# Kernel tuning notes

Hardware: AMD Instinct MI355X
Metric: run time of the kernel (lower is better)

Reference implementation:

```python
import jax, jax.numpy as jnp
import numpy as np

B, T, D = 16384, 3, 512   # batch, task_num, input_dim
G = T + 1                  # expert groups (idx 0 shared)
NE = 4                     # experts per group
H, E = 512, 256            # expert hidden, expert output dim (layers=[512,256])
GH = 256                   # gate hidden
TH, TO = 128, 64           # tower hidden / output dims


def setup_inputs() -> dict:
    key = jax.random.key(0)
    ks = jax.random.split(key, 14)
    s = 0.02
    return {
        "inputs": jax.random.normal(ks[0], (B, G, D), jnp.float32),
        # expert MLPs: [group, expert, ...]
        "expert_W1": jax.random.normal(ks[1], (G, NE, D, H), jnp.float32) * s,
        "expert_b1": jnp.zeros((G, NE, H), jnp.float32),
        "expert_W2": jax.random.normal(ks[2], (G, NE, H, E), jnp.float32) * s,
        "expert_b2": jnp.zeros((G, NE, E), jnp.float32),
        # per-task gates (softmax over G*NE experts)
        "gate_W1": jax.random.normal(ks[3], (T, D, GH), jnp.float32) * s,
        "gate_b1": jnp.zeros((T, GH), jnp.float32),
        "gate_W2": jax.random.normal(ks[4], (T, GH, G * NE), jnp.float32) * s,
        "gate_b2": jnp.zeros((T, G * NE), jnp.float32),
        # per-task towers (is_last=True)
        "tower_W1": jax.random.normal(ks[5], (T, E, TH), jnp.float32) * s,
        "tower_b1": jnp.zeros((T, TH), jnp.float32),
        "tower_W2": jax.random.normal(ks[6], (T, TH, TO), jnp.float32) * s,
        "tower_b2": jnp.zeros((T, TO), jnp.float32),
    }


def reference(inputs, expert_W1, expert_b1, expert_W2, expert_b2,
              gate_W1, gate_b1, gate_W2, gate_b2,
              tower_W1, tower_b1, tower_W2, tower_b2):
    b = inputs.shape[0]
    g, ne = expert_W1.shape[0], expert_W1.shape[1]
    t_num = gate_W1.shape[0]

    # All expert groups in one batched einsum: [B, G, NE, E]
    h1 = jax.nn.relu(jnp.einsum('bgd,gndh->bgnh', inputs, expert_W1) + expert_b1)
    emb = jnp.einsum('bgnh,gnhe->bgne', h1, expert_W2) + expert_b2

    # Task gates on (task input + shared input): softmax over G*NE experts
    gin = inputs[:, 1:, :] + inputs[:, :1, :]                      # [B, T, D]
    gh = jax.nn.relu(jnp.einsum('btd,tdh->bth', gin, gate_W1) + gate_b1)
    gw = jax.nn.softmax(jnp.einsum('bth,thk->btk', gh, gate_W2) + gate_b2, axis=-1)  # [B,T,G*NE]

    emb_sg = jax.lax.stop_gradient(emb)
    group_ids = jnp.arange(g)
    outs = []
    for t in range(t_num):
        # gradient flows only through shared group (0) and own group (t+1)
        keep = (group_ids == 0) | (group_ids == t + 1)              # [G]
        masked = jnp.where(keep[None, :, None, None], emb, emb_sg)  # [B,G,NE,E]
        agg = jnp.einsum('bk,bke->be', gw[:, t], masked.reshape(b, g * ne, -1))  # [B,E]
        th = jax.nn.relu(agg @ tower_W1[t] + tower_b1[t])
        outs.append(th @ tower_W2[t] + tower_b2[t])                 # [B,TO]
    return jnp.concatenate(outs, axis=1)                           # [B, T*TO]
```

## Files before the change

kernel.cpp:

```cpp
#include <hip/hip_runtime.h>
#include <math.h>

#define B_N  16384
#define T_N  3
#define D_N  512
#define G_N  4
#define NE_N 4
#define H_N  512
#define E_N  256
#define GH_N 256
#define K16  16
#define TH_N 128
#define TO_N 64

typedef __attribute__((ext_vector_type(8))) short short8;
typedef __attribute__((ext_vector_type(4))) float floatx4;

__device__ __forceinline__ unsigned short f2bf(float f) {
    union { float f; unsigned u; } v; v.f = f;
    unsigned r = (v.u + 0x7fffu + ((v.u >> 16) & 1u)) >> 16;
    return (unsigned short)r;
}
__device__ __forceinline__ float bf2f(unsigned short h) {
    union { unsigned u; float f; } v; v.u = ((unsigned)h) << 16;
    return v.f;
}
__device__ __forceinline__ unsigned pack2(float lo, float hi) {
    return ((unsigned)f2bf(hi) << 16) | (unsigned)f2bf(lo);
}

typedef const __attribute__((address_space(1))) void gvoid_t;
typedef __attribute__((address_space(3))) void lvoid_t;

#if __has_builtin(__builtin_amdgcn_global_load_lds)
#define HAVE_GLL 1
__device__ __forceinline__ void load_lds16(const void* g, void* l) {
    __builtin_amdgcn_global_load_lds((gvoid_t*)g, (lvoid_t*)l, 16, 0, 0);
}
#else
#define HAVE_GLL 0
#endif

__global__ __launch_bounds__(256) void convert_inputs(
    const float* __restrict__ x, unsigned short* __restrict__ xb,
    unsigned short* __restrict__ ginb)
{
    const long b = blockIdx.x;
    const int tid = threadIdx.x;
    const float* xr = x + b * (G_N * D_N);
    unsigned short* xo = xb + b * (G_N * D_N);
    unsigned short* go = ginb + b * (T_N * D_N);
    float2 v0 = *(const float2*)&xr[tid * 2];
    *(unsigned*)&xo[tid * 2] = pack2(v0.x, v0.y);
    #pragma unroll
    for (int g = 1; g < G_N; ++g) {
        float2 v = *(const float2*)&xr[g * D_N + tid * 2];
        *(unsigned*)&xo[g * D_N + tid * 2] = pack2(v.x, v.y);
        *(unsigned*)&go[(g - 1) * D_N + tid * 2] = pack2(v.x + v0.x, v.y + v0.y);
    }
}

__global__ __launch_bounds__(256) void prep_kernel(
    const float* __restrict__ eW1, const float* __restrict__ eW2,
    const float* __restrict__ gW1, const float* __restrict__ tW1,
    const float* __restrict__ tW2,
    unsigned short* __restrict__ W1t, unsigned short* __restrict__ W2t,
    unsigned short* __restrict__ G1t, unsigned short* __restrict__ TW1t,
    unsigned short* __restrict__ TW2t,
    const float* __restrict__ x, unsigned short* __restrict__ xb,
    unsigned short* __restrict__ ginb)
{
    const int bid = blockIdx.x;
    if (bid < 6648) {
        const float* in; unsigned short* out; int K, N, nx, local;
        if (bid < 4096)      { in = eW1; out = W1t;  K = 512; N = 512; nx = 16; local = bid; }
        else if (bid < 6144) { in = eW2; out = W2t;  K = 512; N = 256; nx = 8;  local = bid - 4096; }
        else if (bid < 6528) { in = gW1; out = G1t;  K = 512; N = 256; nx = 8;  local = bid - 6144; }
        else if (bid < 6624) { in = tW1; out = TW1t; K = 256; N = 128; nx = 4;  local = bid - 6528; }
        else                 { in = tW2; out = TW2t; K = 128; N = 64;  nx = 2;  local = bid - 6624; }
        const int ny = K / 32;
        const int xt = local % nx;
        const int yt = (local / nx) % ny;
        const int z  = local / (nx * ny);
        __shared__ float tile[32][33];
        const int tx = threadIdx.x & 31, ty = threadIdx.x >> 5;
        const long zo = (long)z * K * N;
        const int n0 = xt * 32, k0 = yt * 32;
        #pragma unroll
        for (int i = 0; i < 4; ++i)
            tile[ty + 8 * i][tx] = in[zo + (long)(k0 + ty + 8 * i) * N + n0 + tx];
        __syncthreads();
        #pragma unroll
        for (int i = 0; i < 4; ++i)
            out[zo + (long)(n0 + ty + 8 * i) * K + k0 + tx] = f2bf(tile[tx][ty + 8 * i]);
    } else {
        const long b = bid - 6648;
        const int tid = threadIdx.x;
        const float* xr = x + b * (G_N * D_N);
        unsigned short* xo = xb + b * (G_N * D_N);
        unsigned short* go = ginb + b * (T_N * D_N);
        float2 v0 = *(const float2*)&xr[tid * 2];
        *(unsigned*)&xo[tid * 2] = pack2(v0.x, v0.y);
        #pragma unroll
        for (int g = 1; g < G_N; ++g) {
            float2 v = *(const float2*)&xr[g * D_N + tid * 2];
            *(unsigned*)&xo[g * D_N + tid * 2] = pack2(v.x, v.y);
            *(unsigned*)&go[(g - 1) * D_N + tid * 2] = pack2(v.x + v0.x, v.y + v0.y);
        }
    }
}

__global__ __launch_bounds__(256) void gate_fused(
    const unsigned short* __restrict__ ginb,
    const unsigned short* __restrict__ G1t,
    const float* __restrict__ gb1,
    const float* __restrict__ gW2,
    const float* __restrict__ gb2,
    float* __restrict__ gw)
{
    __shared__ __align__(16) unsigned short sm[40960];
    unsigned short* As  = sm;
    unsigned short* Bs  = sm + 4096;
    unsigned short* w2s = sm;
    unsigned short* ghs = sm + 8192;

    const int tid = threadIdx.x;
    const int t = blockIdx.y;
    const long b0 = (long)blockIdx.x * 128;
    const unsigned short* Ab = ginb + b0 * 1536 + (long)t * 512;

    const int lane16 = tid & 15;
    const int quad = (tid & 63) >> 4;
    const int wave = tid >> 6;
    const int wm = (wave >> 1) * 64;
    const int wn = (wave & 1) * 64;
    const int srow = tid >> 2;
    const int scol = (((tid & 3) ^ ((tid >> 3) & 3)) * 8);
    const int cw8 = ((quad ^ ((lane16 >> 1) & 3)) * 8);

    #pragma unroll
    for (int ncc = 0; ncc < 2; ++ncc) {
        const unsigned short* Bb = G1t + (long)t * 131072 + (long)(ncc * 128) * 512;
        floatx4 acc[4][4] = {};
        for (int k0 = 0; k0 < 512; k0 += 32) {
#if HAVE_GLL
            load_lds16(Ab + (long)srow * 1536 + k0 + scol, &As[tid * 8]);
            load_lds16(Ab + (long)(srow + 64) * 1536 + k0 + scol, &As[2048 + tid * 8]);
            load_lds16(Bb + (long)srow * 512 + k0 + scol, &Bs[tid * 8]);
            load_lds16(Bb + (long)(srow + 64) * 512 + k0 + scol, &Bs[2048 + tid * 8]);
#else
            *(uint4*)&As[tid * 8] = *(const uint4*)(Ab + (long)srow * 1536 + k0 + scol);
            *(uint4*)&As[2048 + tid * 8] = *(const uint4*)(Ab + (long)(srow + 64) * 1536 + k0 + scol);
            *(uint4*)&Bs[tid * 8] = *(const uint4*)(Bb + (long)srow * 512 + k0 + scol);
            *(uint4*)&Bs[2048 + tid * 8] = *(const uint4*)(Bb + (long)(srow + 64) * 512 + k0 + scol);
#endif
            __syncthreads();
            short8 a[4], b[4];
            #pragma unroll
            for (int mi = 0; mi < 4; ++mi)
                a[mi] = *(const short8*)&As[(wm + mi * 16 + lane16) * 32 + cw8];
            #pragma unroll
            for (int ni = 0; ni < 4; ++ni)
                b[ni] = *(const short8*)&Bs[(wn + ni * 16 + lane16) * 32 + cw8];
            #pragma unroll
            for (int mi = 0; mi < 4; ++mi)
                #pragma unroll
                for (int ni = 0; ni < 4; ++ni)
                    acc[mi][ni] = __builtin_amdgcn_mfma_f32_16x16x32_bf16(
                        a[mi], b[ni], acc[mi][ni], 0, 0, 0);
            __syncthreads();
        }
        #pragma unroll
        for (int mi = 0; mi < 4; ++mi) {
            #pragma unroll
            for (int ni = 0; ni < 4; ++ni) {
                const int col = ncc * 128 + wn + ni * 16 + lane16;
                const float bv = gb1[t * GH_N + col];
                #pragma unroll
                for (int r = 0; r < 4; ++r) {
                    const int row = wm + mi * 16 + quad * 4 + r;
                    const int pc = (col & 7) | ((((col >> 3) ^ (row & 7))) << 3);
                    ghs[row * 256 + pc] = f2bf(fmaxf(acc[mi][ni][r] + bv, 0.0f));
                }
            }
        }
    }
    {
        const float* W2p = gW2 + (long)t * (GH_N * K16);
        #pragma unroll
        for (int j = 0; j < 16; ++j)
            w2s[j * 264 + tid] = f2bf(W2p[(long)tid * K16 + j]);
    }
    __syncthreads();

    floatx4 ag[2] = {};
    #pragma unroll
    for (int kk = 0; kk < 8; ++kk) {
        short8 bfr = *(const short8*)&w2s[lane16 * 264 + kk * 32 + quad * 8];
        #pragma unroll
        for (int mi = 0; mi < 2; ++mi) {
            const int row = wave * 32 + mi * 16 + lane16;
            short8 afr = *(const short8*)&ghs[row * 256 + (((kk * 4 + quad) ^ (row & 7)) << 3)];
            ag[mi] = __builtin_amdgcn_mfma_f32_16x16x32_bf16(afr, bfr, ag[mi], 0, 0, 0);
        }
    }

    const float bb2 = gb2[t * K16 + lane16];
    #pragma unroll
    for (int mi = 0; mi < 2; ++mi) {
        float v[4], m = -1e30f;
        #pragma unroll
        for (int r = 0; r < 4; ++r) { v[r] = ag[mi][r] + bb2; }
        #pragma unroll
        for (int r = 0; r < 4; ++r) {
            float mv = v[r];
            #pragma unroll
            for (int d = 1; d < 16; d <<= 1) mv = fmaxf(mv, __shfl_xor(mv, d));
            float e = expf(v[r] - mv);
            float s = e;
            #pragma unroll
            for (int d = 1; d < 16; d <<= 1) s += __shfl_xor(s, d);
            const int row = wave * 32 + mi * 16 + quad * 4 + r;
            gw[(b0 + row) * (T_N * K16) + (long)t * K16 + lane16] = e / s;
        }
    }
}

__global__ __launch_bounds__(256, 2) void expert_fused(
    const unsigned short* __restrict__ xb,
    const unsigned short* __restrict__ W1t,
    const float* __restrict__ eb1,
    const unsigned short* __restrict__ W2t,
    const float* __restrict__ eb2,
    unsigned short* __restrict__ embb)
{
    __shared__ __align__(16) unsigned short sm[33792];
    unsigned short* As  = sm;
    unsigned short* Bs  = sm + 8192;
    unsigned short* h1s = sm + 16384;

    const int tid = threadIdx.x;
    const unsigned bid = blockIdx.x;
    const int e = ((bid & 7) << 1) | ((bid >> 3) & 1);
    const long m0 = (long)(bid >> 4) * 128;
    const int g = e >> 2;

    const unsigned short* Ab  = xb + m0 * 2048 + g * 512;
    const unsigned short* W1b = W1t + (long)e * (512 * 512);
    const unsigned short* W2b = W2t + (long)e * (256 * 512);

    const int lane16 = tid & 15;
    const int quad = (tid & 63) >> 4;
    const int wave = tid >> 6;
    const int wm  = (wave >> 1) * 64;
    const int wn  = (wave & 1) * 64;
    const int wn2 = (wave & 1) * 128;
    const int srow = tid >> 2;
    const int scolsw = (((tid & 3) ^ ((tid >> 3) & 3)) * 8);
    const int cw8 = ((quad ^ ((lane16 >> 1) & 3)) * 8);

    floatx4 acc2[4][8] = {};

    for (int nc = 0; nc < 4; ++nc) {
        const unsigned short* Bb = W1b + ((long)nc << 16);
        floatx4 acc[4][4] = {};
        for (int k0 = 0; k0 < 512; k0 += 64) {
            #pragma unroll
            for (int h = 0; h < 2; ++h) {
                const int kh = k0 + h * 32;
#if HAVE_GLL
                load_lds16(Ab + (long)srow * 2048 + kh + scolsw, &As[h * 4096 + tid * 8]);
                load_lds16(Ab + (long)(srow + 64) * 2048 + kh + scolsw, &As[h * 4096 + 2048 + tid * 8]);
                load_lds16(Bb + (long)srow * 512 + kh + scolsw, &Bs[h * 4096 + tid * 8]);
                load_lds16(Bb + (long)(srow + 64) * 512 + kh + scolsw, &Bs[h * 4096 + 2048 + tid * 8]);
#else
                *(uint4*)&As[h * 4096 + tid * 8] = *(const uint4*)(Ab + (long)srow * 2048 + kh + scolsw);
                *(uint4*)&As[h * 4096 + 2048 + tid * 8] = *(const uint4*)(Ab + (long)(srow + 64) * 2048 + kh + scolsw);
                *(uint4*)&Bs[h * 4096 + tid * 8] = *(const uint4*)(Bb + (long)srow * 512 + kh + scolsw);
                *(uint4*)&Bs[h * 4096 + 2048 + tid * 8] = *(const uint4*)(Bb + (long)(srow + 64) * 512 + kh + scolsw);
#endif
            }
            __syncthreads();
            #pragma unroll
            for (int h = 0; h < 2; ++h) {
                short8 b[4];
                #pragma unroll
                for (int ni = 0; ni < 4; ++ni)
                    b[ni] = *(const short8*)&Bs[h * 4096 + (wn + ni * 16 + lane16) * 32 + cw8];
                #pragma unroll
                for (int mi = 0; mi < 4; ++mi) {
                    short8 a = *(const short8*)&As[h * 4096 + (wm + mi * 16 + lane16) * 32 + cw8];
                    #pragma unroll
                    for (int ni = 0; ni < 4; ++ni)
                        acc[mi][ni] = __builtin_amdgcn_mfma_f32_16x16x32_bf16(
                            a, b[ni], acc[mi][ni], 0, 0, 0);
                }
            }
            __syncthreads();
        }
        #pragma unroll
        for (int mi = 0; mi < 4; ++mi) {
            #pragma unroll
            for (int ni = 0; ni < 4; ++ni) {
                const int col = wn + ni * 16 + lane16;
                const float bv = eb1[e * 512 + nc * 128 + col];
                #pragma unroll
                for (int r = 0; r < 4; ++r) {
                    const int row = wm + mi * 16 + quad * 4 + r;
                    h1s[row * 136 + col] = f2bf(fmaxf(acc[mi][ni][r] + bv, 0.0f));
                }
            }
        }
        __syncthreads();
        #pragma unroll
        for (int ks = 0; ks < 128; ks += 32) {
            #pragma unroll
            for (int i = 0; i < 4; ++i) {
#if HAVE_GLL
                load_lds16(W2b + (long)(srow + 64 * i) * 512 + nc * 128 + ks + scolsw,
                           &As[i * 2048 + tid * 8]);
#else
                *(uint4*)&As[i * 2048 + tid * 8] =
                    *(const uint4*)(W2b + (long)(srow + 64 * i) * 512 + nc * 128 + ks + scolsw);
#endif
            }
            __syncthreads();
            #pragma unroll
            for (int nh = 0; nh < 2; ++nh) {
                short8 b2[4];
                #pragma unroll
                for (int nj = 0; nj < 4; ++nj)
                    b2[nj] = *(const short8*)&As[(wn2 + nh * 64 + nj * 16 + lane16) * 32 + cw8];
                #pragma unroll
                for (int mi = 0; mi < 4; ++mi) {
                    short8 a2 = *(const short8*)&h1s[(wm + mi * 16 + lane16) * 136 + ks + quad * 8];
                    #pragma unroll
                    for (int nj = 0; nj < 4; ++nj)
                        acc2[mi][nh * 4 + nj] = __builtin_amdgcn_mfma_f32_16x16x32_bf16(
                            a2, b2[nj], acc2[mi][nh * 4 + nj], 0, 0, 0);
                }
            }
            __syncthreads();
        }
    }

    unsigned short* Cb = embb + m0 * 4096 + (long)e * 256;
    #pragma unroll
    for (int mi = 0; mi < 4; ++mi) {
        #pragma unroll
        for (int j = 0; j < 8; ++j) {
            const int col = wn2 + (j >> 2) * 64 + (j & 3) * 16 + lane16;
            const float bv = eb2[e * 256 + col];
            #pragma unroll
            for (int r = 0; r < 4; ++r) {
                const int row = wm + mi * 16 + quad * 4 + r;
                Cb[(long)row * 4096 + col] = f2bf(acc2[mi][j][r] + bv);
            }
        }
    }
}

__global__ __launch_bounds__(256) void agg_kernel(
    const unsigned short* __restrict__ emb, const float* __restrict__ gw,
    unsigned short* __restrict__ aggb, long bc)
{
    const long b = (long)blockIdx.x * 8 + (threadIdx.x >> 5);
    const int e0 = (threadIdx.x & 31) * 8;
    const unsigned short* er = emb + b * 4096 + e0;
    const float* gwr = gw + b * 48;
    float a0[8] = {}, a1[8] = {}, a2[8] = {};
    #pragma unroll
    for (int k = 0; k < 16; ++k) {
        short8 v = *(const short8*)(er + (long)k * 256);
        const float w0 = gwr[k], w1 = gwr[16 + k], w2 = gwr[32 + k];
        #pragma unroll
        for (int j = 0; j < 8; ++j) {
            float f = bf2f((unsigned short)v[j]);
            a0[j] += w0 * f; a1[j] += w1 * f; a2[j] += w2 * f;
        }
    }
    unsigned r0[4] = {pack2(a0[0], a0[1]), pack2(a0[2], a0[3]),
                      pack2(a0[4], a0[5]), pack2(a0[6], a0[7])};
    unsigned r1[4] = {pack2(a1[0], a1[1]), pack2(a1[2], a1[3]),
                      pack2(a1[4], a1[5]), pack2(a1[6], a1[7])};
    unsigned r2[4] = {pack2(a2[0], a2[1]), pack2(a2[2], a2[3]),
                      pack2(a2[4], a2[5]), pack2(a2[6], a2[7])};
    *(uint4*)(aggb + 0L * bc * 256 + b * 256 + e0) = *(uint4*)r0;
    *(uint4*)(aggb + 1L * bc * 256 + b * 256 + e0) = *(uint4*)r1;
    *(uint4*)(aggb + 2L * bc * 256 + b * 256 + e0) = *(uint4*)r2;
}

__global__ __launch_bounds__(256) void tower_fused(
    const unsigned short* __restrict__ aggb, long bc,
    const unsigned short* __restrict__ w1t, const float* __restrict__ tb1,
    const unsigned short* __restrict__ w2t, const float* __restrict__ tb2,
    float* __restrict__ out)
{
    __shared__ __align__(16) unsigned short sm[26112];
    unsigned short* As  = sm;
    unsigned short* Bs  = sm + 4096;
    unsigned short* th  = sm;
    unsigned short* w2s = sm + 17408;
    const int tid = threadIdx.x;
    const int t = blockIdx.y;
    const long m0 = (long)blockIdx.x * 128;
    const unsigned short* Ab = aggb + (long)t * bc * 256 + m0 * 256;
    const unsigned short* Bb = w1t + (long)t * (TH_N * E_N);
    const int lane16 = tid & 15;
    const int quad = (tid & 63) >> 4;
    const int wave = tid >> 6;
    const int wm = (wave >> 1) * 64;
    const int wn = (wave & 1) * 64;
    const int srow = tid >> 2;
    const int scolsw = (((tid & 3) ^ ((tid >> 3) & 3)) * 8);
    const int cw8 = ((quad ^ ((lane16 >> 1) & 3)) * 8);

    #pragma unroll
    for (int i = 0; i < 4; ++i) {
        const int seg = i * 256 + tid;
        const int row = seg >> 4, cb = (seg & 15) * 8;
        *(uint4*)&w2s[row * 136 + cb] =
            *(const uint4*)&w2t[(long)t * (TO_N * TH_N) + (long)row * 128 + cb];
    }

    floatx4 acc[4][4] = {};
    for (int k0 = 0; k0 < 256; k0 += 32) {
#if HAVE_GLL
        load_lds16(Ab + (long)srow * 256 + k0 + scolsw, &As[tid * 8]);
        load_lds16(Ab + (long)(srow + 64) * 256 + k0 + scolsw, &As[2048 + tid * 8]);
        load_lds16(Bb + (long)srow * 256 + k0 + scolsw, &Bs[tid * 8]);
        load_lds16(Bb + (long)(srow + 64) * 256 + k0 + scolsw, &Bs[2048 + tid * 8]);
#else
        *(uint4*)&As[tid * 8] = *(const uint4*)(Ab + (long)srow * 256 + k0 + scolsw);
        *(uint4*)&As[2048 + tid * 8] = *(const uint4*)(Ab + (long)(srow + 64) * 256 + k0 + scolsw);
        *(uint4*)&Bs[tid * 8] = *(const uint4*)(Bb + (long)srow * 256 + k0 + scolsw);
        *(uint4*)&Bs[2048 + tid * 8] = *(const uint4*)(Bb + (long)(srow + 64) * 256 + k0 + scolsw);
#endif
        __syncthreads();
        short8 a[4], b[4];
        #pragma unroll
        for (int mi = 0; mi < 4; ++mi)
            a[mi] = *(const short8*)&As[(wm + mi * 16 + lane16) * 32 + cw8];
        #pragma unroll
        for (int ni = 0; ni < 4; ++ni)
            b[ni] = *(const short8*)&Bs[(wn + ni * 16 + lane16) * 32 + cw8];
        #pragma unroll
        for (int mi = 0; mi < 4; ++mi)
            #pragma unroll
            for (int ni = 0; ni < 4; ++ni)
                acc[mi][ni] = __builtin_amdgcn_mfma_f32_16x16x32_bf16(
                    a[mi], b[ni], acc[mi][ni], 0, 0, 0);
        __syncthreads();
    }

    #pragma unroll
    for (int mi = 0; mi < 4; ++mi) {
        #pragma unroll
        for (int ni = 0; ni < 4; ++ni) {
            const int col = wn + ni * 16 + lane16;
            const float bv = tb1[t * TH_N + col];
            #pragma unroll
            for (int r = 0; r < 4; ++r) {
                const int row = wm + mi * 16 + quad * 4 + r;
                th[row * 136 + col] = f2bf(fmaxf(acc[mi][ni][r] + bv, 0.0f));
            }
        }
    }
    __syncthreads();

    floatx4 acc2[2][4] = {};
    #pragma unroll
    for (int kk = 0; kk < 4; ++kk) {
        short8 a2[2], b2[4];
        #pragma unroll
        for (int mi = 0; mi < 2; ++mi)
            a2[mi] = *(const short8*)&th[(wave * 32 + mi * 16 + lane16) * 136 + kk * 32 + quad * 8];
        #pragma unroll
        for (int ni = 0; ni < 4; ++ni)
            b2[ni] = *(const short8*)&w2s[(ni * 16 + lane16) * 136 + kk * 32 + quad * 8];
        #pragma unroll
        for (int mi = 0; mi < 2; ++mi)
            #pragma unroll
            for (int ni = 0; ni < 4; ++ni)
                acc2[mi][ni] = __builtin_amdgcn_mfma_f32_16x16x32_bf16(
                    a2[mi], b2[ni], acc2[mi][ni], 0, 0, 0);
    }
    #pragma unroll
    for (int mi = 0; mi < 2; ++mi) {
        #pragma unroll
        for (int ni = 0; ni < 4; ++ni) {
            const int col = ni * 16 + lane16;
            const float bv = tb2[t * TO_N + col];
            #pragma unroll
            for (int r = 0; r < 4; ++r) {
                const int row = wave * 32 + mi * 16 + quad * 4 + r;
                out[(m0 + row) * (T_N * TO_N) + t * TO_N + col] = acc2[mi][ni][r] + bv;
            }
        }
    }
}

extern "C" void kernel_launch(void* const* d_in, const int* in_sizes, int n_in,
                              void* d_out, int out_size, void* d_ws, size_t ws_size,
                              hipStream_t stream)
{
    const float* x   = (const float*)d_in[0];
    const float* eW1 = (const float*)d_in[1];
    const float* eb1 = (const float*)d_in[2];
    const float* eW2 = (const float*)d_in[3];
    const float* eb2 = (const float*)d_in[4];
    const float* gW1 = (const float*)d_in[5];
    const float* gb1 = (const float*)d_in[6];
    const float* gW2 = (const float*)d_in[7];
    const float* gb2 = (const float*)d_in[8];
    const float* tW1 = (const float*)d_in[9];
    const float* tb1 = (const float*)d_in[10];
    const float* tW2 = (const float*)d_in[11];
    const float* tb2 = (const float*)d_in[12];
    float* out = (float*)d_out;

    char* ws = (char*)d_ws;
    unsigned short* W1t  = (unsigned short*)(ws + 0);
    unsigned short* W2t  = (unsigned short*)(ws + 8388608);
    unsigned short* G1t  = (unsigned short*)(ws + 12582912);
    unsigned short* TW1t = (unsigned short*)(ws + 13369344);
    unsigned short* TW2t = (unsigned short*)(ws + 13565952);
    const size_t WFIX = 13615104;

    long BCo = 0;
    for (long co = 16384; co >= 128; co >>= 1)
        if (WFIX + (size_t)co * 18624 <= ws_size) { BCo = co; break; }
    if (BCo == 0) return;

    char* p = ws + WFIX;
    unsigned short* xb   = (unsigned short*)p; p += BCo * 4096;
    unsigned short* ginb = (unsigned short*)p; p += BCo * 3072;
    unsigned short* embb = (unsigned short*)p; p += BCo * 8192;
    unsigned short* gh   = (unsigned short*)p; p += BCo * 1536;
    float*          gw   = (float*)p;          p += BCo * 192;
    unsigned short* aggb = (unsigned short*)p;
    (void)gh;

    const long n_o = B_N / BCo;

    const long nconv = (n_o == 1) ? BCo : 0;
    prep_kernel<<<dim3((unsigned)(6648 + nconv)), 256, 0, stream>>>(
        eW1, eW2, gW1, tW1, tW2, W1t, W2t, G1t, TW1t, TW2t, x, xb, ginb);

    for (long c = 0; c < n_o; ++c) {
        const float* xc = x + c * BCo * (G_N * D_N);
        float* outc = out + c * BCo * (T_N * TO_N);

        if (n_o > 1)
            convert_inputs<<<BCo, 256, 0, stream>>>(xc, xb, ginb);
        gate_fused<<<dim3(BCo / 128, 3), 256, 0, stream>>>(
            ginb, G1t, gb1, gW2, gb2, gw);
        expert_fused<<<dim3((BCo / 128) * 16), 256, 0, stream>>>(
            xb, W1t, eb1, W2t, eb2, embb);
        agg_kernel<<<BCo / 8, 256, 0, stream>>>(embb, gw, aggb, BCo);
        tower_fused<<<dim3(BCo / 128, 3), 256, 0, stream>>>(
            aggb, BCo, TW1t, tb1, TW2t, tb2, outc);
    }
}
```

Measured before the change: 563.0 us.

## Merge gate and expert kernels into one launch; fuse aggregation into tower

The gate GEMM blocks and the expert MLP blocks now run in a single launch, with the first blocks computing gates, which removes one launch boundary and lets gate work overlap with expert work. The gate kernel is restructured to fit the smaller shared-memory budget by doing its second GEMM per 128-column chunk. The gate-weighted aggregation is folded into the tower kernel, which writes its result directly into LDS and so drops the aggregated-embedding round trip through global memory along with a separate kernel. In exchange, each tower block re-reads the embeddings for each of the three tasks, and the mixed block types may load-balance unevenly.

New measurement: 565.4 us. No clear change (+0.4%).

```diff
diff --git a/kernel.cpp b/kernel.cpp
--- a/kernel.cpp
+++ b/kernel.cpp
@@ -110,154 +110,156 @@
     }
 }
 
-__global__ __launch_bounds__(256) void gate_fused(
+__global__ __launch_bounds__(256, 2) void moe_fused(
+    const unsigned short* __restrict__ xb,
+    const unsigned short* __restrict__ W1t,
+    const float* __restrict__ eb1,
+    const unsigned short* __restrict__ W2t,
+    const float* __restrict__ eb2,
+    unsigned short* __restrict__ embb,
     const unsigned short* __restrict__ ginb,
     const unsigned short* __restrict__ G1t,
     const float* __restrict__ gb1,
     const float* __restrict__ gW2,
     const float* __restrict__ gb2,
-    float* __restrict__ gw)
+    float* __restrict__ gw,
+    int panels)
 {
-    __shared__ __align__(16) unsigned short sm[40960];
-    unsigned short* As  = sm;
-    unsigned short* Bs  = sm + 4096;
-    unsigned short* w2s = sm;
-    unsigned short* ghs = sm + 8192;
-
+    __shared__ __align__(16) unsigned short sm[33792];
     const int tid = threadIdx.x;
-    const int t = blockIdx.y;
-    const long b0 = (long)blockIdx.x * 128;
-    const unsigned short* Ab = ginb + b0 * 1536 + (long)t * 512;
+    const int bid = blockIdx.x;
+    const int nGate = 3 * panels;
 
     const int lane16 = tid & 15;
     const int quad = (tid & 63) >> 4;
     const int wave = tid >> 6;
+    const int srow = tid >> 2;
+    const int scolsw = (((tid & 3) ^ ((tid >> 3) & 3)) * 8);
+    const int cw8 = ((quad ^ ((lane16 >> 1) & 3)) * 8);
     const int wm = (wave >> 1) * 64;
     const int wn = (wave & 1) * 64;
-    const int srow = tid >> 2;
-    const int scol = (((tid & 3) ^ ((tid >> 3) & 3)) * 8);
-    const int cw8 = ((quad ^ ((lane16 >> 1) & 3)) * 8);
-
-    #pragma unroll
-    for (int ncc = 0; ncc < 2; ++ncc) {
-        const unsigned short* Bb = G1t + (long)t * 131072 + (long)(ncc * 128) * 512;
-        floatx4 acc[4][4] = {};
-        for (int k0 = 0; k0 < 512; k0 += 32) {
+
+    if (bid < nGate) {
+        unsigned short* As  = sm;
+        unsigned short* Bs  = sm + 4096;
+        unsigned short* w2s = sm + 8192;
+        unsigned short* ghs = sm + 12416;
+
+        const int t = bid / panels;
+        const long b0 = (long)(bid % panels) * 128;
+        const unsigned short* Ab = ginb + b0 * 1536 + (long)t * 512;
+
+        {
+            const float* W2p = gW2 + (long)t * (GH_N * K16) + (long)tid * K16;
+            float4 w0 = *(const float4*)(W2p);
+            float4 w1 = *(const float4*)(W2p + 4);
+            float4 w2 = *(const float4*)(W2p + 8);
+            float4 w3 = *(const float4*)(W2p + 12);
+            w2s[ 0 * 264 + tid] = f2bf(w0.x); w2s[ 1 * 264 + tid] = f2bf(w0.y);
+            w2s[ 2 * 264 + tid] = f2bf(w0.z); w2s[ 3 * 264 + tid] = f2bf(w0.w);
+            w2s[ 4 * 264 + tid] = f2bf(w1.x); w2s[ 5 * 264 + tid] = f2bf(w1.y);
+            w2s[ 6 * 264 + tid] = f2bf(w1.z); w2s[ 7 * 264 + tid] = f2bf(w1.w);
+            w2s[ 8 * 264 + tid] = f2bf(w2.x); w2s[ 9 * 264 + tid] = f2bf(w2.y);
+            w2s[10 * 264 + tid] = f2bf(w2.z); w2s[11 * 264 + tid] = f2bf(w2.w);
+            w2s[12 * 264 + tid] = f2bf(w3.x); w2s[13 * 264 + tid] = f2bf(w3.y);
+            w2s[14 * 264 + tid] = f2bf(w3.z); w2s[15 * 264 + tid] = f2bf(w3.w);
+        }
+
+        floatx4 ag[2] = {};
+        #pragma unroll
+        for (int ncc = 0; ncc < 2; ++ncc) {
+            const unsigned short* Bb = G1t + (long)t * 131072 + (long)(ncc * 128) * 512;
+            floatx4 acc[4][4] = {};
+            for (int k0 = 0; k0 < 512; k0 += 32) {
 #if HAVE_GLL
-            load_lds16(Ab + (long)srow * 1536 + k0 + scol, &As[tid * 8]);
-            load_lds16(Ab + (long)(srow + 64) * 1536 + k0 + scol, &As[2048 + tid * 8]);
-            load_lds16(Bb + (long)srow * 512 + k0 + scol, &Bs[tid * 8]);
-            load_lds16(Bb + (long)(srow + 64) * 512 + k0 + scol, &Bs[2048 + tid * 8]);
+                load_lds16(Ab + (long)srow * 1536 + k0 + scolsw, &As[tid * 8]);
+                load_lds16(Ab + (long)(srow + 64) * 1536 + k0 + scolsw, &As[2048 + tid * 8]);
+                load_lds16(Bb + (long)srow * 512 + k0 + scolsw, &Bs[tid * 8]);
+                load_lds16(Bb + (long)(srow + 64) * 512 + k0 + scolsw, &Bs[2048 + tid * 8]);
 #else
-            *(uint4*)&As[tid * 8] = *(const uint4*)(Ab + (long)srow * 1536 + k0 + scol);
-            *(uint4*)&As[2048 + tid * 8] = *(const uint4*)(Ab + (long)(srow + 64) * 1536 + k0 + scol);
-            *(uint4*)&Bs[tid * 8] = *(const uint4*)(Bb + (long)srow * 512 + k0 + scol);
-            *(uint4*)&Bs[2048 + tid * 8] = *(const uint4*)(Bb + (long)(srow + 64) * 512 + k0 + scol);
+                *(uint4*)&As[tid * 8] = *(const uint4*)(Ab + (long)srow * 1536 + k0 + scolsw);
+                *(uint4*)&As[2048 + tid * 8] = *(const uint4*)(Ab + (long)(srow + 64) * 1536 + k0 + scolsw);
+                *(uint4*)&Bs[tid * 8] = *(const uint4*)(Bb + (long)srow * 512 + k0 + scolsw);
+                *(uint4*)&Bs[2048 + tid * 8] = *(const uint4*)(Bb + (long)(srow + 64) * 512 + k0 + scolsw);
 #endif
+                __syncthreads();
+                short8 a[4], b[4];
+                #pragma unroll
+                for (int mi = 0; mi < 4; ++mi)
+                    a[mi] = *(const short8*)&As[(wm + mi * 16 + lane16) * 32 + cw8];
+                #pragma unroll
+                for (int ni = 0; ni < 4; ++ni)
+                    b[ni] = *(const short8*)&Bs[(wn + ni * 16 + lane16) * 32 + cw8];
+                #pragma unroll
+                for (int mi = 0; mi < 4; ++mi)
+                    #pragma unroll
+                    for (int ni = 0; ni < 4; ++ni)
+                        acc[mi][ni] = __builtin_amdgcn_mfma_f32_16x16x32_bf16(
+                            a[mi], b[ni], acc[mi][ni], 0, 0, 0);
+                __syncthreads();
+            }
+            #pragma unroll
+            for (int mi = 0; mi < 4; ++mi) {
+                #pragma unroll
+                for (int ni = 0; ni < 4; ++ni) {
+                    const int col = wn + ni * 16 + lane16;
+                    const float bv = gb1[t * GH_N + ncc * 128 + col];
+                    #pragma unroll
+                    for (int r = 0; r < 4; ++r) {
+                        const int row = wm + mi * 16 + quad * 4 + r;
+                        ghs[row * 136 + col] = f2bf(fmaxf(acc[mi][ni][r] + bv, 0.0f));
+                    }
+                }
+            }
             __syncthreads();
-            short8 a[4], b[4];
-            #pragma unroll
-            for (int mi = 0; mi < 4; ++mi)
-                a[mi] = *(const short8*)&As[(wm + mi * 16 + lane16) * 32 + cw8];
-            #pragma unroll
-            for (int ni = 0; ni < 4; ++ni)
-                b[ni] = *(const short8*)&Bs[(wn + ni * 16 + lane16) * 32 + cw8];
-            #pragma unroll
-            for (int mi = 0; mi < 4; ++mi)
-                #pragma unroll
-                for (int ni = 0; ni < 4; ++ni)
-                    acc[mi][ni] = __builtin_amdgcn_mfma_f32_16x16x32_bf16(
-                        a[mi], b[ni], acc[mi][ni], 0, 0, 0);
-            __syncthreads();
-        }
-        #pragma unroll
-        for (int mi = 0; mi < 4; ++mi) {
-            #pragma unroll
-            for (int ni = 0; ni < 4; ++ni) {
-                const int col = ncc * 128 + wn + ni * 16 + lane16;
-                const float bv = gb1[t * GH_N + col];
-                #pragma unroll
-                for (int r = 0; r < 4; ++r) {
-                    const int row = wm + mi * 16 + quad * 4 + r;
-                    const int pc = (col & 7) | ((((col >> 3) ^ (row & 7))) << 3);
-                    ghs[row * 256 + pc] = f2bf(fmaxf(acc[mi][ni][r] + bv, 0.0f));
+            #pragma unroll
+            for (int kk = 0; kk < 4; ++kk) {
+                short8 bfr = *(const short8*)&w2s[lane16 * 264 + ncc * 128 + kk * 32 + quad * 8];
+                #pragma unroll
+                for (int mi = 0; mi < 2; ++mi) {
+                    const int row = wave * 32 + mi * 16 + lane16;
+                    short8 afr = *(const short8*)&ghs[row * 136 + kk * 32 + quad * 8];
+                    ag[mi] = __builtin_amdgcn_mfma_f32_16x16x32_bf16(afr, bfr, ag[mi], 0, 0, 0);
                 }
             }
         }
-    }
-    {
-        const float* W2p = gW2 + (long)t * (GH_N * K16);
-        #pragma unroll
-        for (int j = 0; j < 16; ++j)
-            w2s[j * 264 + tid] = f2bf(W2p[(long)tid * K16 + j]);
-    }
-    __syncthreads();
-
-    floatx4 ag[2] = {};
-    #pragma unroll
-    for (int kk = 0; kk < 8; ++kk) {
-        short8 bfr = *(const short8*)&w2s[lane16 * 264 + kk * 32 + quad * 8];
+
+        const float bb2 = gb2[t * K16 + lane16];
         #pragma unroll
         for (int mi = 0; mi < 2; ++mi) {
-            const int row = wave * 32 + mi * 16 + lane16;
-            short8 afr = *(const short8*)&ghs[row * 256 + (((kk * 4 + quad) ^ (row & 7)) << 3)];
-            ag[mi] = __builtin_amdgcn_mfma_f32_16x16x32_bf16(afr, bfr, ag[mi], 0, 0, 0);
-        }
-    }
-
-    const float bb2 = gb2[t * K16 + lane16];
-    #pragma unroll
-    for (int mi = 0; mi < 2; ++mi) {
-        float v[4], m = -1e30f;
-        #pragma unroll
-        for (int r = 0; r < 4; ++r) { v[r] = ag[mi][r] + bb2; }
-        #pragma unroll
-        for (int r = 0; r < 4; ++r) {
-            float mv = v[r];
-            #pragma unroll
-            for (int d = 1; d < 16; d <<= 1) mv = fmaxf(mv, __shfl_xor(mv, d));
-            float e = expf(v[r] - mv);
-            float s = e;
-            #pragma unroll
-            for (int d = 1; d < 16; d <<= 1) s += __shfl_xor(s, d);
-            const int row = wave * 32 + mi * 16 + quad * 4 + r;
-            gw[(b0 + row) * (T_N * K16) + (long)t * K16 + lane16] = e / s;
-        }
-    }
-}
-
-__global__ __launch_bounds__(256, 2) void expert_fused(
-    const unsigned short* __restrict__ xb,
-    const unsigned short* __restrict__ W1t,
-    const float* __restrict__ eb1,
-    const unsigned short* __restrict__ W2t,
-    const float* __restrict__ eb2,
-    unsigned short* __restrict__ embb)
-{
-    __shared__ __align__(16) unsigned short sm[33792];
+            float v[4];
+            #pragma unroll
+            for (int r = 0; r < 4; ++r) v[r] = ag[mi][r] + bb2;
+            #pragma unroll
+            for (int r = 0; r < 4; ++r) {
+                float mv = v[r];
+                #pragma unroll
+                for (int d = 1; d < 16; d <<= 1) mv = fmaxf(mv, __shfl_xor(mv, d));
+                float e = expf(v[r] - mv);
+                float s = e;
+                #pragma unroll
+                for (int d = 1; d < 16; d <<= 1) s += __shfl_xor(s, d);
+                const int row = wave * 32 + mi * 16 + quad * 4 + r;
+                gw[(b0 + row) * (T_N * K16) + (long)t * K16 + lane16] = e / s;
+            }
+        }
+        return;
+    }
+
     unsigned short* As  = sm;
     unsigned short* Bs  = sm + 8192;
     unsigned short* h1s = sm + 16384;
 
-    const int tid = threadIdx.x;
-    const unsigned bid = blockIdx.x;
-    const int e = ((bid & 7) << 1) | ((bid >> 3) & 1);
-    const long m0 = (long)(bid >> 4) * 128;
+    const unsigned ebid = bid - nGate;
+    const int e = ((ebid & 7) << 1) | ((ebid >> 3) & 1);
+    const long m0 = (long)(ebid >> 4) * 128;
     const int g = e >> 2;
 
     const unsigned short* Ab  = xb + m0 * 2048 + g * 512;
     const unsigned short* W1b = W1t + (long)e * (512 * 512);
     const unsigned short* W2b = W2t + (long)e * (256 * 512);
 
-    const int lane16 = tid & 15;
-    const int quad = (tid & 63) >> 4;
-    const int wave = tid >> 6;
-    const int wm  = (wave >> 1) * 64;
-    const int wn  = (wave & 1) * 64;
     const int wn2 = (wave & 1) * 128;
-    const int srow = tid >> 2;
-    const int scolsw = (((tid & 3) ^ ((tid >> 3) & 3)) * 8);
-    const int cw8 = ((quad ^ ((lane16 >> 1) & 3)) * 8);
 
     floatx4 acc2[4][8] = {};
 
@@ -360,52 +362,19 @@
     }
 }
 
-__global__ __launch_bounds__(256) void agg_kernel(
-    const unsigned short* __restrict__ emb, const float* __restrict__ gw,
-    unsigned short* __restrict__ aggb, long bc)
-{
-    const long b = (long)blockIdx.x * 8 + (threadIdx.x >> 5);
-    const int e0 = (threadIdx.x & 31) * 8;
-    const unsigned short* er = emb + b * 4096 + e0;
-    const float* gwr = gw + b * 48;
-    float a0[8] = {}, a1[8] = {}, a2[8] = {};
-    #pragma unroll
-    for (int k = 0; k < 16; ++k) {
-        short8 v = *(const short8*)(er + (long)k * 256);
-        const float w0 = gwr[k], w1 = gwr[16 + k], w2 = gwr[32 + k];
-        #pragma unroll
-        for (int j = 0; j < 8; ++j) {
-            float f = bf2f((unsigned short)v[j]);
-            a0[j] += w0 * f; a1[j] += w1 * f; a2[j] += w2 * f;
-        }
-    }
-    unsigned r0[4] = {pack2(a0[0], a0[1]), pack2(a0[2], a0[3]),
-                      pack2(a0[4], a0[5]), pack2(a0[6], a0[7])};
-    unsigned r1[4] = {pack2(a1[0], a1[1]), pack2(a1[2], a1[3]),
-                      pack2(a1[4], a1[5]), pack2(a1[6], a1[7])};
-    unsigned r2[4] = {pack2(a2[0], a2[1]), pack2(a2[2], a2[3]),
-                      pack2(a2[4], a2[5]), pack2(a2[6], a2[7])};
-    *(uint4*)(aggb + 0L * bc * 256 + b * 256 + e0) = *(uint4*)r0;
-    *(uint4*)(aggb + 1L * bc * 256 + b * 256 + e0) = *(uint4*)r1;
-    *(uint4*)(aggb + 2L * bc * 256 + b * 256 + e0) = *(uint4*)r2;
-}
-
-__global__ __launch_bounds__(256) void tower_fused(
-    const unsigned short* __restrict__ aggb, long bc,
-    const unsigned short* __restrict__ w1t, const float* __restrict__ tb1,
-    const unsigned short* __restrict__ w2t, const float* __restrict__ tb2,
+__global__ __launch_bounds__(256) void agg_tower(
+    const unsigned short* __restrict__ embb,
+    const float* __restrict__ gw,
+    const unsigned short* __restrict__ w1t,
+    const float* __restrict__ tb1,
+    const unsigned short* __restrict__ w2t,
+    const float* __restrict__ tb2,
     float* __restrict__ out)
 {
-    __shared__ __align__(16) unsigned short sm[26112];
-    unsigned short* As  = sm;
-    unsigned short* Bs  = sm + 4096;
-    unsigned short* th  = sm;
-    unsigned short* w2s = sm + 17408;
+    __shared__ __align__(16) unsigned short sm[37888];
     const int tid = threadIdx.x;
     const int t = blockIdx.y;
-    const long m0 = (long)blockIdx.x * 128;
-    const unsigned short* Ab = aggb + (long)t * bc * 256 + m0 * 256;
-    const unsigned short* Bb = w1t + (long)t * (TH_N * E_N);
+    const long b0 = (long)blockIdx.x * 128;
     const int lane16 = tid & 15;
     const int quad = (tid & 63) >> 4;
     const int wave = tid >> 6;
@@ -415,6 +384,84 @@
     const int scolsw = (((tid & 3) ^ ((tid >> 3) & 3)) * 8);
     const int cw8 = ((quad ^ ((lane16 >> 1) & 3)) * 8);
 
+    float* gws = (float*)(sm + 33792);
+    {
+        const int r = tid >> 1, j0 = (tid & 1) * 8;
+        const float* gp = gw + (b0 + r) * (T_N * K16) + (long)t * K16 + j0;
+        *(float4*)&gws[r * 16 + j0]     = *(const float4*)gp;
+        *(float4*)&gws[r * 16 + j0 + 4] = *(const float4*)(gp + 4);
+    }
+    __syncthreads();
+
+    {
+        const int gidx = tid & 31;
+        const int r0 = tid >> 5;
+        const int col8 = gidx * 8;
+        #pragma unroll
+        for (int i = 0; i < 16; ++i) {
+            const int row = r0 + 8 * i;
+            const unsigned short* er = embb + (b0 + row) * 4096 + col8;
+            float a8[8] = {};
+            #pragma unroll
+            for (int k = 0; k < 16; ++k) {
+                short8 v = *(const short8*)(er + (long)k * 256);
+                const float w = gws[row * 16 + k];
+                #pragma unroll
+                for (int j = 0; j < 8; ++j) a8[j] += w * bf2f((unsigned short)v[j]);
+            }
+            unsigned rr[4] = {pack2(a8[0], a8[1]), pack2(a8[2], a8[3]),
+                              pack2(a8[4], a8[5]), pack2(a8[6], a8[7])};
+            *(uint4*)&sm[row * 264 + ((gidx ^ (row & 7)) * 8)] = *(uint4*)rr;
+        }
+    }
+    __syncthreads();
+
+    unsigned short* Bs = sm + 33792;
+    const unsigned short* Bb = w1t + (long)t * (TH_N * E_N);
+    floatx4 acc[4][4] = {};
+    for (int k0 = 0; k0 < 256; k0 += 32) {
+#if HAVE_GLL
+        load_lds16(Bb + (long)srow * 256 + k0 + scolsw, &Bs[tid * 8]);
+        load_lds16(Bb + (long)(srow + 64) * 256 + k0 + scolsw, &Bs[2048 + tid * 8]);
+#else
+        *(uint4*)&Bs[tid * 8] = *(const uint4*)(Bb + (long)srow * 256 + k0 + scolsw);
+        *(uint4*)&Bs[2048 + tid * 8] = *(const uint4*)(Bb + (long)(srow + 64) * 256 + k0 + scolsw);
+#endif
+        __syncthreads();
+        short8 a[4], b[4];
+        #pragma unroll
+        for (int mi = 0; mi < 4; ++mi) {
+            const int row = wm + mi * 16 + lane16;
+            const int gg = ((k0 >> 3) + quad) ^ (row & 7);
+            a[mi] = *(const short8*)&sm[row * 264 + gg * 8];
+        }
+        #pragma unroll
+        for (int ni = 0; ni < 4; ++ni)
+            b[ni] = *(const short8*)&Bs[(wn + ni * 16 + lane16) * 32 + cw8];
+        #pragma unroll
+        for (int mi = 0; mi < 4; ++mi)
+            #pragma unroll
+            for (int ni = 0; ni < 4; ++ni)
+                acc[mi][ni] = __builtin_amdgcn_mfma_f32_16x16x32_bf16(
+                    a[mi], b[ni], acc[mi][ni], 0, 0, 0);
+        __syncthreads();
+    }
+
+    unsigned short* th  = sm;
+    unsigned short* w2s = sm + 17408;
+    #pragma unroll
+    for (int mi = 0; mi < 4; ++mi) {
+        #pragma unroll
+        for (int ni = 0; ni < 4; ++ni) {
+            const int col = wn + ni * 16 + lane16;
+            const float bv = tb1[t * TH_N + col];
+            #pragma unroll
+            for (int r = 0; r < 4; ++r) {
+                const int row = wm + mi * 16 + quad * 4 + r;
+                th[row * 136 + col] = f2bf(fmaxf(acc[mi][ni][r] + bv, 0.0f));
+            }
+        }
+    }
     #pragma unroll
     for (int i = 0; i < 4; ++i) {
         const int seg = i * 256 + tid;
@@ -422,50 +469,6 @@
         *(uint4*)&w2s[row * 136 + cb] =
             *(const uint4*)&w2t[(long)t * (TO_N * TH_N) + (long)row * 128 + cb];
     }
-
-    floatx4 acc[4][4] = {};
-    for (int k0 = 0; k0 < 256; k0 += 32) {
-#if HAVE_GLL
-        load_lds16(Ab + (long)srow * 256 + k0 + scolsw, &As[tid * 8]);
-        load_lds16(Ab + (long)(srow + 64) * 256 + k0 + scolsw, &As[2048 + tid * 8]);
-        load_lds16(Bb + (long)srow * 256 + k0 + scolsw, &Bs[tid * 8]);
-        load_lds16(Bb + (long)(srow + 64) * 256 + k0 + scolsw, &Bs[2048 + tid * 8]);
-#else
-        *(uint4*)&As[tid * 8] = *(const uint4*)(Ab + (long)srow * 256 + k0 + scolsw);
-        *(uint4*)&As[2048 + tid * 8] = *(const uint4*)(Ab + (long)(srow + 64) * 256 + k0 + scolsw);
-        *(uint4*)&Bs[tid * 8] = *(const uint4*)(Bb + (long)srow * 256 + k0 + scolsw);
-        *(uint4*)&Bs[2048 + tid * 8] = *(const uint4*)(Bb + (long)(srow + 64) * 256 + k0 + scolsw);
-#endif
-        __syncthreads();
-        short8 a[4], b[4];
-        #pragma unroll
-        for (int mi = 0; mi < 4; ++mi)
-            a[mi] = *(const short8*)&As[(wm + mi * 16 + lane16) * 32 + cw8];
-        #pragma unroll
-        for (int ni = 0; ni < 4; ++ni)
-            b[ni] = *(const short8*)&Bs[(wn + ni * 16 + lane16) * 32 + cw8];
-        #pragma unroll
-        for (int mi = 0; mi < 4; ++mi)
-            #pragma unroll
-            for (int ni = 0; ni < 4; ++ni)
-                acc[mi][ni] = __builtin_amdgcn_mfma_f32_16x16x32_bf16(
-                    a[mi], b[ni], acc[mi][ni], 0, 0, 0);
-        __syncthreads();
-    }
-
-    #pragma unroll
-    for (int mi = 0; mi < 4; ++mi) {
-        #pragma unroll
-        for (int ni = 0; ni < 4; ++ni) {
-            const int col = wn + ni * 16 + lane16;
-            const float bv = tb1[t * TH_N + col];
-            #pragma unroll
-            for (int r = 0; r < 4; ++r) {
-                const int row = wm + mi * 16 + quad * 4 + r;
-                th[row * 136 + col] = f2bf(fmaxf(acc[mi][ni][r] + bv, 0.0f));
-            }
-        }
-    }
     __syncthreads();
 
     floatx4 acc2[2][4] = {};
@@ -494,7 +497,7 @@
             #pragma unroll
             for (int r = 0; r < 4; ++r) {
                 const int row = wave * 32 + mi * 16 + quad * 4 + r;
-                out[(m0 + row) * (T_N * TO_N) + t * TO_N + col] = acc2[mi][ni][r] + bv;
+                out[(b0 + row) * (T_N * TO_N) + t * TO_N + col] = acc2[mi][ni][r] + bv;
             }
         }
     }
@@ -536,12 +539,11 @@
     unsigned short* xb   = (unsigned short*)p; p += BCo * 4096;
     unsigned short* ginb = (unsigned short*)p; p += BCo * 3072;
     unsigned short* embb = (unsigned short*)p; p += BCo * 8192;
-    unsigned short* gh   = (unsigned short*)p; p += BCo * 1536;
+    p += BCo * 1536;
     float*          gw   = (float*)p;          p += BCo * 192;
-    unsigned short* aggb = (unsigned short*)p;
-    (void)gh;
 
     const long n_o = B_N / BCo;
+    const int panels = (int)(BCo / 128);
 
     const long nconv = (n_o == 1) ? BCo : 0;
     prep_kernel<<<dim3((unsigned)(6648 + nconv)), 256, 0, stream>>>(
@@ -553,12 +555,10 @@
 
         if (n_o > 1)
             convert_inputs<<<BCo, 256, 0, stream>>>(xc, xb, ginb);
-        gate_fused<<<dim3(BCo / 128, 3), 256, 0, stream>>>(
-            ginb, G1t, gb1, gW2, gb2, gw);
-        expert_fused<<<dim3((BCo / 128) * 16), 256, 0, stream>>>(
-            xb, W1t, eb1, W2t, eb2, embb);
-        agg_kernel<<<BCo / 8, 256, 0, stream>>>(embb, gw, aggb, BCo);
-        tower_fused<<<dim3(BCo / 128, 3), 256, 0, stream>>>(
-            aggb, BCo, TW1t, tb1, TW2t, tb2, outc);
-    }
-}
+        moe_fused<<<dim3((unsigned)(panels * 19)), 256, 0, stream>>>(
+            xb, W1t, eb1, W2t, eb2, embb,
+            ginb, G1t, gb1, gW2, gb2, gw, panels);
+        agg_tower<<<dim3(panels, 3), 256, 0, stream>>>(
+            embb, gw, TW1t, tb1, TW2t, tb2, outc);
+    }
+}
```
